# Kernel tuning notes

Hardware: AMD Instinct MI355X
Metric: run time of the kernel (lower is better)

Reference implementation:

```python
import jax, jax.numpy as jnp
import numpy as np

B, T, C, H, D = 2, 2048, 768, 12, 64
ATTN_MULT = 0.125  # 1/sqrt(head_dim)


def setup_inputs() -> dict:
    key = jax.random.key(0)
    k0, k1, k2 = jax.random.split(key, 3)
    x = jax.random.normal(k0, (B, T, C), jnp.float32)
    w_attn = jax.random.normal(k1, (3 * H * D, C), jnp.float32) * 0.02
    b_attn = jnp.zeros((3 * H * D,), jnp.float32)
    w_proj = jax.random.normal(k2, (C, H * D), jnp.float32) * 0.02
    b_proj = jnp.zeros((C,), jnp.float32)
    return {"x": x, "w_attn": w_attn, "b_attn": b_attn, "w_proj": w_proj, "b_proj": b_proj}


def reference(x, w_attn, b_attn, w_proj, b_proj):
    Bx, Tx, Cx = x.shape
    # fused qkv projection (torch nn.Linear: x @ W^T + b)
    qkv = x @ w_attn.T + b_attn                      # [B,T,3*H*D]
    q, k, v = jnp.split(qkv, 3, axis=2)
    def to_heads(t):
        return t.reshape(Bx, Tx, H, D).transpose(0, 2, 1, 3)  # [B,H,T,D]
    q, k, v = to_heads(q), to_heads(k), to_heads(v)
    att = jnp.einsum('bhqd,bhkd->bhqk', q, k) * ATTN_MULT     # [B,H,T,T]

    causal = jnp.tril(jnp.ones((Tx, Tx), dtype=bool))
    # selection scores from head 0 (selective attention)
    S = jax.nn.relu(att[:, 0])                                # [B,T,T]
    # prevent_from_masking_myself: zero diagonal; protect_bos_token: zero key col 0
    smask = causal & ~jnp.eye(Tx, dtype=bool)
    smask = smask.at[:, 0].set(False)
    S = jnp.where(smask, S, 0.0)
    # exclusive cumulative sum over the query dim: F[i,j] = sum_{i'<i} S[i',j]
    Fmask = jnp.cumsum(S, axis=-2) - S                        # [B,T,T]
    att = att - Fmask[:, None]                                # broadcast over heads

    att = jnp.where(causal, att, -jnp.inf)
    p = jax.nn.softmax(att, axis=-1)                          # [B,H,T,T]
    y = jnp.einsum('bhqk,bhkd->bhqd', p, v)                   # [B,H,T,D]
    y = y.transpose(0, 2, 1, 3).reshape(Bx, Tx, H * D)
    return y @ w_proj.T + b_proj
```

## Files before the change

### kernel.cpp

```cpp
#include <hip/hip_runtime.h>
#include <hip/hip_bf16.h>

#define BB 2
#define TT 2048
#define CC 768
#define HH 12
#define DD 64
#define NQKV 2304
#define MTOT (BB*TT)
#define CH 32
#define NCH (TT/CH)

typedef __bf16 bf16x8 __attribute__((ext_vector_type(8)));
typedef __bf16 bf16x4 __attribute__((ext_vector_type(4)));
typedef float  f32x4  __attribute__((ext_vector_type(4)));

__device__ __forceinline__ f32x4 mfma16(bf16x8 a, bf16x8 b, f32x4 c) {
    return __builtin_amdgcn_mfma_f32_16x16x32_bf16(a, b, c, 0, 0, 0);
}

__device__ __forceinline__ void load_lds16(const void* g, void* l) {
    __builtin_amdgcn_global_load_lds(
        (const __attribute__((address_space(1))) void*)g,
        (__attribute__((address_space(3))) void*)l, 16, 0, 0);
}

__global__ __launch_bounds__(256) void cvt_bf16_kernel(
    const float* __restrict__ x, const float* __restrict__ wa, const float* __restrict__ wp,
    __bf16* __restrict__ xb, __bf16* __restrict__ wab, __bf16* __restrict__ wpb)
{
    const long NX = (long)MTOT * CC;
    const long NWA = (long)NQKV * CC;
    long idx = ((long)blockIdx.x * 256 + threadIdx.x) * 4;
    const float* src; __bf16* dst; long off;
    if (idx < NX)            { src = x;  dst = xb;  off = idx; }
    else if (idx < NX + NWA) { src = wa; dst = wab; off = idx - NX; }
    else                     { src = wp; dst = wpb; off = idx - NX - NWA; }
    float4 v = *(const float4*)(src + off);
    bf16x4 o;
    o[0] = (__bf16)v.x; o[1] = (__bf16)v.y; o[2] = (__bf16)v.z; o[3] = (__bf16)v.w;
    *(bf16x4*)(dst + off) = o;
}

template<int EPI>
__global__ __launch_bounds__(256, 2) void gemm_nt_kernel(
    const __bf16* __restrict__ A, const __bf16* __restrict__ Bw,
    const float* __restrict__ bias,
    __bf16* __restrict__ oBF, float* __restrict__ oF32, int K)
{
    __shared__ __align__(16) __bf16 As[128 * 32];
    __shared__ __align__(16) __bf16 Bs[128 * 32];
    const int tid = threadIdx.x;
    const int m0 = blockIdx.y * 128, n0 = blockIdx.x * 128;
    const int w = tid >> 6, lane = tid & 63, quad = lane >> 4, l16 = lane & 15;
    const int wm = (w >> 1) * 64, wn = (w & 1) * 64;
    const int grow = w * 16 + (lane >> 2);
    const int gcol = (lane & 3) * 8;
    __bf16* AsW = As + w * 512;
    __bf16* BsW = Bs + w * 512;

    f32x4 acc[4][4] = {};

    for (int kt = 0; kt < K; kt += 32) {
        __syncthreads();
        load_lds16(A  + (long)(m0 + grow) * K + kt + gcol,      AsW);
        load_lds16(A  + (long)(m0 + grow + 64) * K + kt + gcol, AsW + 2048);
        load_lds16(Bw + (long)(n0 + grow) * K + kt + gcol,      BsW);
        load_lds16(Bw + (long)(n0 + grow + 64) * K + kt + gcol, BsW + 2048);
        __syncthreads();

        bf16x8 af[4], bfr[4];
#pragma unroll
        for (int g = 0; g < 4; g++)  af[g]  = *(const bf16x8*)(As + (wm + g * 16 + l16) * 32 + quad * 8);
#pragma unroll
        for (int jb = 0; jb < 4; jb++) bfr[jb] = *(const bf16x8*)(Bs + (wn + jb * 16 + l16) * 32 + quad * 8);
#pragma unroll
        for (int g = 0; g < 4; g++)
#pragma unroll
            for (int jb = 0; jb < 4; jb++)
                acc[g][jb] = mfma16(af[g], bfr[jb], acc[g][jb]);
    }

    const int ldc = (EPI == 0) ? NQKV : CC;
#pragma unroll
    for (int jb = 0; jb < 4; jb++) {
        const int n = n0 + wn + jb * 16 + l16;
        const float bv = bias[n];
#pragma unroll
        for (int g = 0; g < 4; g++) {
#pragma unroll
            for (int r = 0; r < 4; r++) {
                const int m = m0 + wm + g * 16 + quad * 4 + r;
                const float v = acc[g][jb][r] + bv;
                if (EPI == 0) oBF[(long)m * ldc + n] = (__bf16)v;
                else          oF32[(long)m * ldc + n] = v;
            }
        }
    }
}

__global__ __launch_bounds__(256) void transpose_v_kernel(
    const __bf16* __restrict__ qkv, __bf16* __restrict__ vT)
{
    __shared__ __bf16 Tl[64][72];
    const int tt = blockIdx.x, h = blockIdx.y, b = blockIdx.z;
    const int tid = threadIdx.x;
    const int r8 = tid >> 3, c8 = (tid & 7) * 8;
    const __bf16* src = qkv + (long)(b * TT + tt * 64) * NQKV + 1536 + h * 64;
#pragma unroll
    for (int p = 0; p < 2; p++) {
        const int row = p * 32 + r8;
        bf16x8 v = *(const bf16x8*)(src + (long)row * NQKV + c8);
#pragma unroll
        for (int e = 0; e < 8; e++) Tl[c8 + e][row] = v[e];
    }
    __syncthreads();
    __bf16* dst = vT + ((long)(b * HH + h) << 6) * TT + tt * 64;
#pragma unroll
    for (int p = 0; p < 2; p++) {
        const int d = p * 32 + r8;
        *(bf16x8*)(dst + (long)d * TT + c8) = *(const bf16x8*)(&Tl[d][c8]);
    }
}

__global__ __launch_bounds__(256) void sgemm_kernel(
    const __bf16* __restrict__ qkv, __bf16* __restrict__ S)
{
    const int tj = blockIdx.x, ti = blockIdx.y, b = blockIdx.z;
    if (tj > ti) return;
    const int w = threadIdx.x >> 6, lane = threadIdx.x & 63, quad = lane >> 4, l16 = lane & 15;
    const int i0 = ti * 64 + w * 16;

    const __bf16* qp = qkv + (long)(b * TT + i0 + l16) * NQKV + quad * 8;
    bf16x8 a0 = *(const bf16x8*)qp, a1 = *(const bf16x8*)(qp + 32);
    const __bf16* kbase = qkv + (long)(b * TT) * NQKV + 768;

#pragma unroll
    for (int jb = 0; jb < 4; jb++) {
        const __bf16* kp = kbase + (long)(tj * 64 + jb * 16 + l16) * NQKV + quad * 8;
        bf16x8 b0 = *(const bf16x8*)kp, b1 = *(const bf16x8*)(kp + 32);
        f32x4 acc = {};
        acc = mfma16(a0, b0, acc);
        acc = mfma16(a1, b1, acc);
        const int j = tj * 64 + jb * 16 + l16;
#pragma unroll
        for (int r = 0; r < 4; r++) {
            const int i = i0 + quad * 4 + r;
            float v = fmaxf(acc[r] * 0.125f, 0.0f);
            v = (j >= 1 && j < i) ? v : 0.0f;
            S[((long)b * TT + i) * TT + j] = (__bf16)v;
        }
    }
}

__global__ __launch_bounds__(256) void scan_sum_kernel(
    const __bf16* __restrict__ S, float* __restrict__ csum)
{
    const int j = blockIdx.x * 256 + threadIdx.x;
    const int chunk = blockIdx.y, b = blockIdx.z;
    const int ib = chunk * CH;
    const __bf16* p = S + ((long)b * TT + ib) * TT + j;
    float s = 0.0f;
#pragma unroll
    for (int ii = 0; ii < CH; ii++) {
        float v = (float)p[(long)ii * TT];
        s += ((ib + ii) > j) ? v : 0.0f;
    }
    csum[(b * NCH + chunk) * TT + j] = s;
}

__global__ __launch_bounds__(256) void scan_write_kernel(
    const __bf16* __restrict__ S, const float* __restrict__ csum, __bf16* __restrict__ Fo)
{
    const int j = blockIdx.x * 256 + threadIdx.x;
    const int chunk = blockIdx.y, b = blockIdx.z;
    const int ib = chunk * CH;
    float off = 0.0f;
    for (int c = 0; c < chunk; c++) off += csum[(b * NCH + c) * TT + j];
    const __bf16* ps = S  + ((long)b * TT + ib) * TT + j;
    __bf16*       pf = Fo + ((long)b * TT + ib) * TT + j;
#pragma unroll
    for (int ii = 0; ii < CH; ii++) {
        float v = ((ib + ii) > j) ? (float)ps[(long)ii * TT] : 0.0f;
        pf[(long)ii * TT] = (__bf16)off;
        off += v;
    }
}

__global__ __launch_bounds__(128, 2) void flash_kernel(
    const __bf16* __restrict__ qkv, const __bf16* __restrict__ vT,
    const __bf16* __restrict__ F, __bf16* __restrict__ y)
{
    __shared__ __align__(16) __bf16 Ks[2][64 * 64];
    __shared__ __align__(16) __bf16 Vs[2][64 * 64];
    __shared__ __align__(16) __bf16 Pls[2][16 * 72];
    const int bid = blockIdx.x, h = blockIdx.y, b = blockIdx.z;
    const int w = threadIdx.x >> 6, lane = threadIdx.x & 63, quad = lane >> 4, l16 = lane & 15;
    const int rl = lane >> 3;
    const int cs8 = ((lane & 7) ^ rl) * 8;
    const int sw0 = ((quad)     ^ (l16 & 7)) * 8;
    const int sw1 = ((quad + 4) ^ (l16 & 7)) * 8;
    __bf16* Pl = &Pls[w][0];
    const __bf16* kb = qkv + (long)(b * TT) * NQKV + 768 + h * 64;
    const __bf16* vb = vT + ((long)(b * HH + h) << 6) * TT;
    const __bf16* Fbase = F + (long)b * TT * TT;

    const int qt0 = bid, qt1 = 63 - bid;
    const int n0 = (qt0 >> 1) + 1, n1 = (qt1 >> 1) + 1;
    const int N = n0 + n1;

    int i0 = qt0 * 32 + w * 16;
    const __bf16* qp = qkv + (long)(b * TT + i0 + l16) * NQKV + h * 64 + quad * 8;
    bf16x8 aq0 = *(const bf16x8*)qp;
    bf16x8 aq1 = *(const bf16x8*)(qp + 32);

    f32x4 O[4] = {};
    float lr[4] = {0.0f, 0.0f, 0.0f, 0.0f};
    __bf16 Fn[4][4];

    {
        __bf16* KsW = Ks[0] + w * 2048;
        __bf16* VsW = Vs[0] + w * 2048;
#pragma unroll
        for (int t = 0; t < 4; t++)
            load_lds16(kb + (long)(w * 32 + t * 8 + rl) * NQKV + cs8, KsW + t * 512);
#pragma unroll
        for (int t = 0; t < 4; t++)
            load_lds16(vb + (long)(w * 32 + t * 8 + rl) * TT + cs8, VsW + t * 512);
        const __bf16* Fb = Fbase + (long)i0 * TT;
#pragma unroll
        for (int jh = 0; jh < 4; jh++)
#pragma unroll
            for (int r = 0; r < 4; r++)
                Fn[jh][r] = Fb[(long)(quad * 4 + r) * TT + jh * 16 + l16];
    }

    for (int it = 0; it < N; it++) {
        const int ph = (it >= n0);
        const int jt = (it - (ph ? n0 : 0)) << 6;
        const int qt = ph ? qt1 : qt0;
        const int jtend = (qt >> 1) << 6;

        __syncthreads();

        __bf16 Fc[4][4];
#pragma unroll
        for (int jh = 0; jh < 4; jh++)
#pragma unroll
            for (int r = 0; r < 4; r++)
                Fc[jh][r] = Fn[jh][r];

        if (it + 1 < N) {
            const int ph2 = (it + 1 >= n0);
            const int jt2 = ((it + 1) - (ph2 ? n0 : 0)) << 6;
            __bf16* KsW = Ks[(it + 1) & 1] + w * 2048;
            __bf16* VsW = Vs[(it + 1) & 1] + w * 2048;
#pragma unroll
            for (int t = 0; t < 4; t++)
                load_lds16(kb + (long)(jt2 + w * 32 + t * 8 + rl) * NQKV + cs8, KsW + t * 512);
#pragma unroll
            for (int t = 0; t < 4; t++)
                load_lds16(vb + (long)(w * 32 + t * 8 + rl) * TT + jt2 + cs8, VsW + t * 512);
            const int i0n = (ph2 ? qt1 : qt0) * 32 + w * 16;
            const __bf16* Fb2 = Fbase + (long)i0n * TT;
#pragma unroll
            for (int jh = 0; jh < 4; jh++)
#pragma unroll
                for (int r = 0; r < 4; r++)
                    Fn[jh][r] = Fb2[(long)(quad * 4 + r) * TT + jt2 + jh * 16 + l16];
        }
        __builtin_amdgcn_sched_barrier(0);

        const __bf16* Kc = Ks[it & 1];
        const __bf16* Vc = Vs[it & 1];
        float sc[4][4];
#pragma unroll
        for (int jh = 0; jh < 4; jh++) {
            const int jr = jh * 16 + l16;
            const bf16x8 kc0 = *(const bf16x8*)(Kc + (jr << 6) + sw0);
            const bf16x8 kc1 = *(const bf16x8*)(Kc + (jr << 6) + sw1);
            f32x4 acc = {};
            acc = mfma16(aq0, kc0, acc);
            acc = mfma16(aq1, kc1, acc);
#pragma unroll
            for (int r = 0; r < 4; r++) sc[jh][r] = acc[r];
        }
        if (jt == jtend) {
#pragma unroll
            for (int jh = 0; jh < 4; jh++) {
                const int j = jt + jh * 16 + l16;
#pragma unroll
                for (int r = 0; r < 4; r++) {
                    const int i = i0 + quad * 4 + r;
                    float v = fmaf(sc[jh][r], 0.125f, -(float)Fc[jh][r]);
                    v = (j <= i) ? v : -35.0f;
                    const float p = __expf(v);
                    sc[jh][r] = p;
                    lr[r] += p;
                }
            }
        } else {
#pragma unroll
            for (int jh = 0; jh < 4; jh++) {
#pragma unroll
                for (int r = 0; r < 4; r++) {
                    float v = fmaf(sc[jh][r], 0.125f, -(float)Fc[jh][r]);
                    const float p = __expf(v);
                    sc[jh][r] = p;
                    lr[r] += p;
                }
            }
        }
#pragma unroll
        for (int r = 0; r < 4; r++) {
            const int il = quad * 4 + r;
#pragma unroll
            for (int jh = 0; jh < 4; jh++)
                Pl[il * 72 + jh * 16 + l16] = (__bf16)sc[jh][r];
        }
        const bf16x8 ap0 = *(const bf16x8*)(Pl + l16 * 72 + quad * 8);
        const bf16x8 ap1 = *(const bf16x8*)(Pl + l16 * 72 + 32 + quad * 8);
#pragma unroll
        for (int db = 0; db < 4; db++) {
            const bf16x8 vv0 = *(const bf16x8*)(Vc + ((db * 16 + l16) << 6) + sw0);
            const bf16x8 vv1 = *(const bf16x8*)(Vc + ((db * 16 + l16) << 6) + sw1);
            O[db] = mfma16(ap0, vv0, O[db]);
            O[db] = mfma16(ap1, vv1, O[db]);
        }
        if (jt == jtend) {
            float inv[4];
#pragma unroll
            for (int r = 0; r < 4; r++) {
                float s = lr[r];
#pragma unroll
                for (int off = 8; off >= 1; off >>= 1) s += __shfl_xor(s, off, 16);
                inv[r] = 1.0f / s;
            }
#pragma unroll
            for (int db = 0; db < 4; db++) {
#pragma unroll
                for (int r = 0; r < 4; r++) {
                    const int i = i0 + quad * 4 + r;
                    y[((long)(b * TT + i)) * (HH * DD) + h * 64 + db * 16 + l16] = (__bf16)(O[db][r] * inv[r]);
                }
            }
#pragma unroll
            for (int db = 0; db < 4; db++) { O[db][0] = 0.f; O[db][1] = 0.f; O[db][2] = 0.f; O[db][3] = 0.f; }
            lr[0] = lr[1] = lr[2] = lr[3] = 0.0f;
            if (!ph) {
                i0 = qt1 * 32 + w * 16;
                const __bf16* qp2 = qkv + (long)(b * TT + i0 + l16) * NQKV + h * 64 + quad * 8;
                aq0 = *(const bf16x8*)qp2;
                aq1 = *(const bf16x8*)(qp2 + 32);
            }
        }
    }
}

extern "C" void kernel_launch(void* const* d_in, const int* in_sizes, int n_in,
                              void* d_out, int out_size, void* d_ws, size_t ws_size,
                              hipStream_t stream)
{
    const float* x      = (const float*)d_in[0];
    const float* w_attn = (const float*)d_in[1];
    const float* b_attn = (const float*)d_in[2];
    const float* w_proj = (const float*)d_in[3];
    const float* b_proj = (const float*)d_in[4];
    float* out = (float*)d_out;

    char* ws = (char*)d_ws;
    __bf16* xb   = (__bf16*)ws; ws += (long)MTOT * CC * 2;
    __bf16* wab  = (__bf16*)ws; ws += (long)NQKV * CC * 2;
    __bf16* wpb  = (__bf16*)ws; ws += (long)CC * (HH*DD) * 2;
    __bf16* qkvb = (__bf16*)ws; ws += (long)MTOT * NQKV * 2;
    __bf16* vtb  = (__bf16*)ws; ws += (long)BB * HH * TT * DD * 2;
    __bf16* SF   = (__bf16*)ws; ws += (long)BB * TT * TT * 2;
    __bf16* Fo   = (__bf16*)ws; ws += (long)BB * TT * TT * 2;
    float*  cs   = (float*)ws;  ws += (long)BB * NCH * TT * 4;
    __bf16* yb   = (__bf16*)ws; ws += (long)MTOT * (HH*DD) * 2;

    cvt_bf16_kernel<<<5376, 256, 0, stream>>>(x, w_attn, w_proj, xb, wab, wpb);
    gemm_nt_kernel<0><<<dim3(NQKV / 128, MTOT / 128), 256, 0, stream>>>(
        xb, wab, b_attn, qkvb, nullptr, CC);
    transpose_v_kernel<<<dim3(TT / 64, HH, BB), 256, 0, stream>>>(qkvb, vtb);
    sgemm_kernel<<<dim3(TT / 64, TT / 64, BB), 256, 0, stream>>>(qkvb, SF);
    scan_sum_kernel<<<dim3(TT / 256, NCH, BB), 256, 0, stream>>>(SF, cs);
    scan_write_kernel<<<dim3(TT / 256, NCH, BB), 256, 0, stream>>>(SF, cs, Fo);
    flash_kernel<<<dim3(32, HH, BB), 128, 0, stream>>>(qkvb, vtb, Fo, yb);
    gemm_nt_kernel<1><<<dim3(CC / 128, MTOT / 128), 256, 0, stream>>>(
        yb, wpb, b_proj, nullptr, out, HH * DD);
}
```

Baseline: 228.1 us.

## Fuse column chunk sums into S gemm with atomics and swizzle flash grid

The S-matrix kernel now reduces each 32-row chunk's column sums with wave shuffles and atomically adds them into csum. This removes the separate scan_sum pass over S, at the cost of a memset plus atomics. scan_write skips column blocks that lie entirely above the causal diagonal. The flash kernel uses a 1D grid with a swizzled mapping of block id to (batch, head, tile), intended to group work for better cache locality.

```diff
diff --git a/kernel.cpp b/kernel.cpp
--- a/kernel.cpp
+++ b/kernel.cpp
@@ -124,12 +124,13 @@
 }
 
 __global__ __launch_bounds__(256) void sgemm_kernel(
-    const __bf16* __restrict__ qkv, __bf16* __restrict__ S)
+    const __bf16* __restrict__ qkv, __bf16* __restrict__ S, float* __restrict__ csum)
 {
     const int tj = blockIdx.x, ti = blockIdx.y, b = blockIdx.z;
     if (tj > ti) return;
     const int w = threadIdx.x >> 6, lane = threadIdx.x & 63, quad = lane >> 4, l16 = lane & 15;
     const int i0 = ti * 64 + w * 16;
+    const int chunk = ti * 2 + (w >> 1);
 
     const __bf16* qp = qkv + (long)(b * TT + i0 + l16) * NQKV + quad * 8;
     bf16x8 a0 = *(const bf16x8*)qp, a1 = *(const bf16x8*)(qp + 32);
@@ -143,40 +144,32 @@
         acc = mfma16(a0, b0, acc);
         acc = mfma16(a1, b1, acc);
         const int j = tj * 64 + jb * 16 + l16;
+        float colsum = 0.0f;
 #pragma unroll
         for (int r = 0; r < 4; r++) {
             const int i = i0 + quad * 4 + r;
             float v = fmaxf(acc[r] * 0.125f, 0.0f);
             v = (j >= 1 && j < i) ? v : 0.0f;
             S[((long)b * TT + i) * TT + j] = (__bf16)v;
-        }
-    }
-}
-
-__global__ __launch_bounds__(256) void scan_sum_kernel(
-    const __bf16* __restrict__ S, float* __restrict__ csum)
-{
-    const int j = blockIdx.x * 256 + threadIdx.x;
+            colsum += v;
+        }
+        colsum += __shfl_xor(colsum, 16);
+        colsum += __shfl_xor(colsum, 32);
+        if (quad == 0)
+            atomicAdd(&csum[((long)b * NCH + chunk) * TT + j], colsum);
+    }
+}
+
+__global__ __launch_bounds__(256) void scan_write_kernel(
+    const __bf16* __restrict__ S, const float* __restrict__ csum, __bf16* __restrict__ Fo)
+{
     const int chunk = blockIdx.y, b = blockIdx.z;
     const int ib = chunk * CH;
-    const __bf16* p = S + ((long)b * TT + ib) * TT + j;
-    float s = 0.0f;
-#pragma unroll
-    for (int ii = 0; ii < CH; ii++) {
-        float v = (float)p[(long)ii * TT];
-        s += ((ib + ii) > j) ? v : 0.0f;
-    }
-    csum[(b * NCH + chunk) * TT + j] = s;
-}
-
-__global__ __launch_bounds__(256) void scan_write_kernel(
-    const __bf16* __restrict__ S, const float* __restrict__ csum, __bf16* __restrict__ Fo)
-{
-    const int j = blockIdx.x * 256 + threadIdx.x;
-    const int chunk = blockIdx.y, b = blockIdx.z;
-    const int ib = chunk * CH;
+    const int j0 = blockIdx.x * 256;
+    if (j0 >= ib + CH) return;
+    const int j = j0 + threadIdx.x;
     float off = 0.0f;
-    for (int c = 0; c < chunk; c++) off += csum[(b * NCH + c) * TT + j];
+    for (int c = 0; c < chunk; c++) off += csum[((long)b * NCH + c) * TT + j];
     const __bf16* ps = S  + ((long)b * TT + ib) * TT + j;
     __bf16*       pf = Fo + ((long)b * TT + ib) * TT + j;
 #pragma unroll
@@ -194,7 +187,11 @@
     __shared__ __align__(16) __bf16 Ks[2][64 * 64];
     __shared__ __align__(16) __bf16 Vs[2][64 * 64];
     __shared__ __align__(16) __bf16 Pls[2][16 * 72];
-    const int bid = blockIdx.x, h = blockIdx.y, b = blockIdx.z;
+    const int gid = blockIdx.x;
+    const int xs = gid & 7, s = gid >> 3;
+    const int gi = xs + ((s >> 5) << 3);
+    const int bid = s & 31;
+    const int h = gi % 12, b = gi / 12;
     const int w = threadIdx.x >> 6, lane = threadIdx.x & 63, quad = lane >> 4, l16 = lane & 15;
     const int rl = lane >> 3;
     const int cs8 = ((lane & 7) ^ rl) * 8;
@@ -331,10 +328,10 @@
             float inv[4];
 #pragma unroll
             for (int r = 0; r < 4; r++) {
-                float s = lr[r];
-#pragma unroll
-                for (int off = 8; off >= 1; off >>= 1) s += __shfl_xor(s, off, 16);
-                inv[r] = 1.0f / s;
+                float s2 = lr[r];
+#pragma unroll
+                for (int off = 8; off >= 1; off >>= 1) s2 += __shfl_xor(s2, off, 16);
+                inv[r] = 1.0f / s2;
             }
 #pragma unroll
             for (int db = 0; db < 4; db++) {
@@ -379,14 +376,14 @@
     float*  cs   = (float*)ws;  ws += (long)BB * NCH * TT * 4;
     __bf16* yb   = (__bf16*)ws; ws += (long)MTOT * (HH*DD) * 2;
 
+    hipMemsetAsync(cs, 0, (long)BB * NCH * TT * 4, stream);
     cvt_bf16_kernel<<<5376, 256, 0, stream>>>(x, w_attn, w_proj, xb, wab, wpb);
     gemm_nt_kernel<0><<<dim3(NQKV / 128, MTOT / 128), 256, 0, stream>>>(
         xb, wab, b_attn, qkvb, nullptr, CC);
     transpose_v_kernel<<<dim3(TT / 64, HH, BB), 256, 0, stream>>>(qkvb, vtb);
-    sgemm_kernel<<<dim3(TT / 64, TT / 64, BB), 256, 0, stream>>>(qkvb, SF);
-    scan_sum_kernel<<<dim3(TT / 256, NCH, BB), 256, 0, stream>>>(SF, cs);
+    sgemm_kernel<<<dim3(TT / 64, TT / 64, BB), 256, 0, stream>>>(qkvb, SF, cs);
     scan_write_kernel<<<dim3(TT / 256, NCH, BB), 256, 0, stream>>>(SF, cs, Fo);
-    flash_kernel<<<dim3(32, HH, BB), 128, 0, stream>>>(qkvb, vtb, Fo, yb);
+    flash_kernel<<<dim3(768), 128, 0, stream>>>(qkvb, vtb, Fo, yb);
     gemm_nt_kernel<1><<<dim3(CC / 128, MTOT / 128), 256, 0, stream>>>(
         yb, wpb, b_proj, nullptr, out, HH * DD);
 }
```

Result: faster. 221.5 us (-2.9%).
